# Performance work log

Measured on AMD Instinct MI355X. Metric: run time of the kernel, lower is better.

Reference implementation:

```python
import jax, jax.numpy as jnp
import numpy as np

B, S, E, H = 2, 2048, 1024, 16
D = E // H  # head_dim = 64
SCALE = D ** -0.5


def setup_inputs() -> dict:
    key = jax.random.key(0)
    ks = jax.random.split(key, 5)
    std = E ** -0.5
    return {
        "x": jax.random.normal(ks[0], (B, S, E), dtype=jnp.float32),
        "wq": jax.random.normal(ks[1], (E, E), dtype=jnp.float32) * std,
        "wk": jax.random.normal(ks[2], (E, E), dtype=jnp.float32) * std,
        "wv": jax.random.normal(ks[3], (E, E), dtype=jnp.float32) * std,
        "wo": jax.random.normal(ks[4], (E, E), dtype=jnp.float32) * std,
    }


def reference(x, wq, wk, wv, wo):
    b, s, e = x.shape
    # nn.Linear(bias=False): y = x @ W.T; then split heads -> [B,H,S,D]
    def heads(w):
        return jnp.einsum('bse,fe->bsf', x, w).reshape(b, s, H, D).transpose(0, 2, 1, 3)
    q, k, v = heads(wq), heads(wk), heads(wv)
    attn = jnp.einsum('bhqd,bhkd->bhqk', q, k) * SCALE  # [B,H,S,S]
    attn = jax.nn.softmax(attn, axis=-1)
    out = jnp.einsum('bhqk,bhkd->bhqd', attn, v)        # [B,H,S,D]
    out = out.transpose(0, 2, 1, 3).reshape(b, s, e)
    return jnp.einsum('bse,fe->bsf', out, wo)
```

## Files before the change

### kernel.cpp

```cpp
#include <hip/hip_runtime.h>
#include <stdint.h>

typedef unsigned short ushort_t;
typedef __bf16 bfx8 __attribute__((ext_vector_type(8), may_alias));
typedef __bf16 bfx2 __attribute__((ext_vector_type(2), may_alias));
typedef unsigned short usx8 __attribute__((ext_vector_type(8), may_alias));
typedef unsigned int uix2 __attribute__((ext_vector_type(2), may_alias));
typedef unsigned int uix4 __attribute__((ext_vector_type(4), may_alias));
typedef float f32x4 __attribute__((ext_vector_type(4)));
typedef float f32x4m __attribute__((ext_vector_type(4), may_alias));
typedef float f32x16 __attribute__((ext_vector_type(16)));

#define BB 2
#define SS 2048
#define EE 1024
#define HH 16
#define DD 64
#define MM (BB * SS)
#define XN ((size_t)MM * EE)
#define WN ((size_t)EE * EE)
#define QSCALE 0.18033688011112042f

__device__ __forceinline__ unsigned short f2bf(float f) {
  unsigned int u = __builtin_bit_cast(unsigned int, f);
  u += 0x7fffu + ((u >> 16) & 1u);
  return (unsigned short)(u >> 16);
}

__device__ __forceinline__ usx8 cvt8(const float* p) {
  f32x4m a = *(const f32x4m*)p;
  f32x4m b = *(const f32x4m*)(p + 4);
  usx8 r;
  r[0] = f2bf(a[0]); r[1] = f2bf(a[1]); r[2] = f2bf(a[2]); r[3] = f2bf(a[3]);
  r[4] = f2bf(b[0]); r[5] = f2bf(b[1]); r[6] = f2bf(b[2]); r[7] = f2bf(b[3]);
  return r;
}

__device__ __forceinline__ unsigned int pk2(float lo, float hi) {
  bfx2 t;
  t[0] = (__bf16)lo;
  t[1] = (__bf16)hi;
  return __builtin_bit_cast(unsigned int, t);
}

__device__ __forceinline__ void gl_lds16(const ushort_t* g, ushort_t* l) {
  __builtin_amdgcn_global_load_lds(
      (const __attribute__((address_space(1))) unsigned int*)g,
      (__attribute__((address_space(3))) unsigned int*)l, 16, 0, 0);
}

__global__ __launch_bounds__(256)
void cvt_qkv(const float* __restrict__ x, const float* __restrict__ wq,
             const float* __restrict__ wk, const float* __restrict__ wv,
             ushort_t* __restrict__ dst) {
  size_t i8 = ((size_t)blockIdx.x * 256 + threadIdx.x) * 8;
  const float* s;
  size_t off;
  if (i8 < XN)               { s = x;  off = i8; }
  else if (i8 < XN + WN)     { s = wq; off = i8 - XN; }
  else if (i8 < XN + 2 * WN) { s = wk; off = i8 - XN - WN; }
  else                       { s = wv; off = i8 - XN - 2 * WN; }
  *(usx8*)(dst + i8) = cvt8(s + off);
}

__global__ __launch_bounds__(256)
void cvt_one(const float* __restrict__ s, ushort_t* __restrict__ dst) {
  size_t i8 = ((size_t)blockIdx.x * 256 + threadIdx.x) * 8;
  *(usx8*)(dst + i8) = cvt8(s + i8);
}

__global__ __launch_bounds__(256)
void gemm_qkv(const ushort_t* __restrict__ xb,
              const ushort_t* __restrict__ wqb, const ushort_t* __restrict__ wkb,
              const ushort_t* __restrict__ wvb,
              ushort_t* __restrict__ Qb, ushort_t* __restrict__ Kb,
              ushort_t* __restrict__ Vtb) {
  __shared__ ushort_t As[128 * 32];
  __shared__ ushort_t Bs[128 * 32];

  const int bid = blockIdx.x;
  const ushort_t *A, *W;
  ushort_t* C;
  int bx, by, N;
  float scale = 1.0f;
  if (bid < 512) {
    int t = bid & 255;
    bx = t & 7;  by = t >> 3;
    A = xb;  N = EE;
    if (bid < 256) { W = wqb; C = Qb; scale = QSCALE; }
    else           { W = wkb; C = Kb; }
  } else {
    int t = bid - 512;
    bx = t & 31; by = t >> 5;
    A = wvb; W = xb; C = Vtb; N = MM;
  }
  const int K = EE;

  const int tid = threadIdx.x;
  const int lane = tid & 63;
  const int w = tid >> 6;
  const int l15 = lane & 15, l16 = lane >> 4;
  const int m0 = by * 128;
  const int n0 = bx * 128;
  const int wr = w >> 1, wc = w & 1;

  f32x4 acc[4][4];
#pragma unroll
  for (int i = 0; i < 4; ++i)
#pragma unroll
    for (int j = 0; j < 4; ++j)
#pragma unroll
      for (int r = 0; r < 4; ++r) acc[i][j][r] = 0.0f;

  for (int k0 = 0; k0 < K; k0 += 32) {
#pragma unroll
    for (int q = 0; q < 2; ++q) {
      int c = w * 128 + q * 64 + lane;
      int row = c >> 2, col = c & 3;
      gl_lds16(A + (size_t)(m0 + row) * K + k0 + col * 8,
               As + (size_t)(w * 128 + q * 64) * 8);
      gl_lds16(W + (size_t)(n0 + row) * K + k0 + col * 8,
               Bs + (size_t)(w * 128 + q * 64) * 8);
    }
    __syncthreads();

    bfx8 af[4], bfr[4];
#pragma unroll
    for (int i = 0; i < 4; ++i) {
      int mr = wr * 64 + i * 16 + l15;
      af[i] = *(const bfx8*)(As + mr * 32 + l16 * 8);
      int nr = wc * 64 + i * 16 + l15;
      bfr[i] = *(const bfx8*)(Bs + nr * 32 + l16 * 8);
    }
#pragma unroll
    for (int i = 0; i < 4; ++i)
#pragma unroll
      for (int j = 0; j < 4; ++j)
        acc[i][j] = __builtin_amdgcn_mfma_f32_16x16x32_bf16(af[i], bfr[j],
                                                            acc[i][j], 0, 0, 0);
    __syncthreads();
  }

#pragma unroll
  for (int i = 0; i < 4; ++i) {
    int mr = m0 + wr * 64 + i * 16 + l16 * 4;
#pragma unroll
    for (int j = 0; j < 4; ++j) {
      int nc = n0 + wc * 64 + j * 16 + l15;
#pragma unroll
      for (int r = 0; r < 4; ++r)
        C[(size_t)(mr + r) * N + nc] = f2bf(acc[i][j][r] * scale);
    }
  }
}

__global__ __launch_bounds__(256)
void gemm_o(const ushort_t* __restrict__ A, const ushort_t* __restrict__ W,
            float* __restrict__ C, int M, int N, int K) {
  __shared__ ushort_t As[128 * 32];
  __shared__ ushort_t Bs[128 * 32];

  const int tid = threadIdx.x;
  const int lane = tid & 63;
  const int w = tid >> 6;
  const int l15 = lane & 15, l16 = lane >> 4;
  const int m0 = blockIdx.y * 128;
  const int n0 = blockIdx.x * 128;
  const int wr = w >> 1, wc = w & 1;

  f32x4 acc[4][4];
#pragma unroll
  for (int i = 0; i < 4; ++i)
#pragma unroll
    for (int j = 0; j < 4; ++j)
#pragma unroll
      for (int r = 0; r < 4; ++r) acc[i][j][r] = 0.0f;

  for (int k0 = 0; k0 < K; k0 += 32) {
#pragma unroll
    for (int q = 0; q < 2; ++q) {
      int c = w * 128 + q * 64 + lane;
      int row = c >> 2, col = c & 3;
      gl_lds16(A + (size_t)(m0 + row) * K + k0 + col * 8,
               As + (size_t)(w * 128 + q * 64) * 8);
      gl_lds16(W + (size_t)(n0 + row) * K + k0 + col * 8,
               Bs + (size_t)(w * 128 + q * 64) * 8);
    }
    __syncthreads();

    bfx8 af[4], bfr[4];
#pragma unroll
    for (int i = 0; i < 4; ++i) {
      int mr = wr * 64 + i * 16 + l15;
      af[i] = *(const bfx8*)(As + mr * 32 + l16 * 8);
      int nr = wc * 64 + i * 16 + l15;
      bfr[i] = *(const bfx8*)(Bs + nr * 32 + l16 * 8);
    }
#pragma unroll
    for (int i = 0; i < 4; ++i)
#pragma unroll
      for (int j = 0; j < 4; ++j)
        acc[i][j] = __builtin_amdgcn_mfma_f32_16x16x32_bf16(af[i], bfr[j],
                                                            acc[i][j], 0, 0, 0);
    __syncthreads();
  }

#pragma unroll
  for (int i = 0; i < 4; ++i) {
    int mr = m0 + wr * 64 + i * 16 + l16 * 4;
#pragma unroll
    for (int j = 0; j < 4; ++j) {
      int nc = n0 + wc * 64 + j * 16 + l15;
#pragma unroll
      for (int r = 0; r < 4; ++r)
        C[(size_t)(mr + r) * N + nc] = acc[i][j][r];
    }
  }
}

__global__ __launch_bounds__(128)
void attn_fwd(const ushort_t* Q, const ushort_t* __restrict__ Kg,
              const ushort_t* __restrict__ Vt_g, ushort_t* AO) {
  __shared__ ushort_t Ks[64 * 72];
  __shared__ ushort_t Vs[64 * 72];

  const int tid = threadIdx.x;
  const int lane = tid & 63;
  const int w = tid >> 6;
  const int l31 = lane & 31, hi = lane >> 5;
  const int qt = blockIdx.x, h = blockIdx.y, b = blockIdx.z;
  const int q0 = qt * 64 + w * 32;

  bfx8 bq[4];
#pragma unroll
  for (int t = 0; t < 4; ++t)
    bq[t] = *(const bfx8*)(Q + (size_t)(b * SS + q0 + l31) * EE + h * DD +
                           t * 16 + hi * 8);

  f32x16 o0, o1;
#pragma unroll
  for (int r = 0; r < 16; ++r) { o0[r] = 0.0f; o1[r] = 0.0f; }
  float lsum = 0.0f;

  int cr[4], cc[4];
#pragma unroll
  for (int i = 0; i < 4; ++i) {
    int c = tid + i * 128;
    cr[i] = c >> 3;
    cc[i] = c & 7;
  }
  const ushort_t* kbase = Kg + (size_t)b * SS * EE + h * DD;
  const ushort_t* vbase = Vt_g + (size_t)h * DD * MM + (size_t)b * SS;

  usx8 kreg[4], vreg[4];
#pragma unroll
  for (int i = 0; i < 4; ++i) {
    kreg[i] = *(const usx8*)(kbase + (size_t)cr[i] * EE + cc[i] * 8);
    vreg[i] = *(const usx8*)(vbase + (size_t)cr[i] * MM + cc[i] * 8);
  }

  for (int kt = 0; kt < SS; kt += 64) {
    __syncthreads();
#pragma unroll
    for (int i = 0; i < 4; ++i) {
      *(usx8*)(Ks + cr[i] * 72 + cc[i] * 8) = kreg[i];
      *(usx8*)(Vs + cr[i] * 72 + cc[i] * 8) = vreg[i];
    }
    __syncthreads();
    if (kt + 64 < SS) {
#pragma unroll
      for (int i = 0; i < 4; ++i) {
        kreg[i] =
            *(const usx8*)(kbase + (size_t)(kt + 64 + cr[i]) * EE + cc[i] * 8);
        vreg[i] =
            *(const usx8*)(vbase + (size_t)cr[i] * MM + kt + 64 + cc[i] * 8);
      }
    }

    f32x16 pa, pb;
#pragma unroll
    for (int r = 0; r < 16; ++r) { pa[r] = 0.0f; pb[r] = 0.0f; }
#pragma unroll
    for (int t = 0; t < 4; ++t) {
      bfx8 ak0 = *(const bfx8*)(Ks + l31 * 72 + t * 16 + hi * 8);
      bfx8 ak1 = *(const bfx8*)(Ks + (32 + l31) * 72 + t * 16 + hi * 8);
      pa = __builtin_amdgcn_mfma_f32_32x32x16_bf16(ak0, bq[t], pa, 0, 0, 0);
      pb = __builtin_amdgcn_mfma_f32_32x32x16_bf16(ak1, bq[t], pb, 0, 0, 0);
    }

#pragma unroll
    for (int r = 0; r < 16; ++r) {
      pa[r] = __builtin_exp2f(pa[r]);
      pb[r] = __builtin_exp2f(pb[r]);
      lsum += pa[r] + pb[r];
    }

    unsigned int dwA[8], dwB[8];
#pragma unroll
    for (int s = 0; s < 8; ++s) {
      dwA[s] = pk2(pa[2 * s], pa[2 * s + 1]);
      dwB[s] = pk2(pb[2 * s], pb[2 * s + 1]);
    }
    bfx8 fd[4];
#pragma unroll
    for (int g = 0; g < 2; ++g) {
      auto sA = __builtin_amdgcn_permlane32_swap(dwA[4 * g + 0], dwA[4 * g + 2],
                                                 false, false);
      auto sB = __builtin_amdgcn_permlane32_swap(dwA[4 * g + 1], dwA[4 * g + 3],
                                                 false, false);
      uix4 f;
      f[0] = sA[0]; f[1] = sB[0]; f[2] = sA[1]; f[3] = sB[1];
      fd[g] = __builtin_bit_cast(bfx8, f);
      auto tA = __builtin_amdgcn_permlane32_swap(dwB[4 * g + 0], dwB[4 * g + 2],
                                                 false, false);
      auto tB = __builtin_amdgcn_permlane32_swap(dwB[4 * g + 1], dwB[4 * g + 3],
                                                 false, false);
      uix4 f2;
      f2[0] = tA[0]; f2[1] = tB[0]; f2[2] = tA[1]; f2[3] = tB[1];
      fd[2 + g] = __builtin_bit_cast(bfx8, f2);
    }

#pragma unroll
    for (int kk = 0; kk < 4; ++kk) {
      bfx8 av0 = *(const bfx8*)(Vs + l31 * 72 + kk * 16 + hi * 8);
      bfx8 av1 = *(const bfx8*)(Vs + (32 + l31) * 72 + kk * 16 + hi * 8);
      o0 = __builtin_amdgcn_mfma_f32_32x32x16_bf16(av0, fd[kk], o0, 0, 0, 0);
      o1 = __builtin_amdgcn_mfma_f32_32x32x16_bf16(av1, fd[kk], o1, 0, 0, 0);
    }
  }

  lsum += __shfl_xor(lsum, 32);
  float inv = 1.0f / lsum;

  ushort_t* orow = AO + (size_t)(b * SS + q0 + l31) * EE + h * DD;
#pragma unroll
  for (int g = 0; g < 4; ++g) {
    uix2 s0, s1;
    s0[0] = pk2(o0[4 * g + 0] * inv, o0[4 * g + 1] * inv);
    s0[1] = pk2(o0[4 * g + 2] * inv, o0[4 * g + 3] * inv);
    *(uix2*)(orow + 8 * g + 4 * hi) = s0;
    s1[0] = pk2(o1[4 * g + 0] * inv, o1[4 * g + 1] * inv);
    s1[1] = pk2(o1[4 * g + 2] * inv, o1[4 * g + 3] * inv);
    *(uix2*)(orow + 32 + 8 * g + 4 * hi) = s1;
  }
}

extern "C" void kernel_launch(void* const* d_in, const int* in_sizes, int n_in,
                              void* d_out, int out_size, void* d_ws, size_t ws_size,
                              hipStream_t stream) {
  const float* x  = (const float*)d_in[0];
  const float* wq = (const float*)d_in[1];
  const float* wk = (const float*)d_in[2];
  const float* wv = (const float*)d_in[3];
  const float* wo = (const float*)d_in[4];
  float* out = (float*)d_out;

  ushort_t* Qb  = (ushort_t*)d_ws;
  ushort_t* Kb  = Qb + XN;
  ushort_t* Vtb = Kb + XN;
  ushort_t* Ab  = Qb;
  ushort_t* S    = (ushort_t*)d_out;
  ushort_t* xb   = S;
  ushort_t* wqb  = S + XN;
  ushort_t* wkb  = S + XN + WN;
  ushort_t* wvb  = S + XN + 2 * WN;
  ushort_t* wob  = Kb;

  dim3 blk(256);
  cvt_qkv<<<dim3((unsigned)((XN + 3 * WN) / (256 * 8))), blk, 0, stream>>>(
      x, wq, wk, wv, S);
  gemm_qkv<<<dim3(768), blk, 0, stream>>>(xb, wqb, wkb, wvb, Qb, Kb, Vtb);
  attn_fwd<<<dim3(SS / 64, HH, BB), dim3(128), 0, stream>>>(Qb, Kb, Vtb, Ab);
  cvt_one<<<dim3((unsigned)(WN / (256 * 8))), blk, 0, stream>>>(wo, wob);
  gemm_o<<<dim3(EE / 128, MM / 128), blk, 0, stream>>>(
      Ab, wob, out, MM, EE, EE);
}
```

Measured before the change: 212.4 us.

## Load attention K/V fragments directly from global memory, dropping LDS staging

```diff
diff --git a/kernel.cpp b/kernel.cpp
--- a/kernel.cpp
+++ b/kernel.cpp
@@ -218,18 +218,16 @@
   }
 }
 
-__global__ __launch_bounds__(128)
+__global__ __launch_bounds__(64)
 void attn_fwd(const ushort_t* Q, const ushort_t* __restrict__ Kg,
               const ushort_t* __restrict__ Vt_g, ushort_t* AO) {
-  __shared__ ushort_t Ks[64 * 72];
-  __shared__ ushort_t Vs[64 * 72];
-
-  const int tid = threadIdx.x;
-  const int lane = tid & 63;
-  const int w = tid >> 6;
+  const int lane = threadIdx.x;
   const int l31 = lane & 31, hi = lane >> 5;
   const int qt = blockIdx.x, h = blockIdx.y, b = blockIdx.z;
-  const int q0 = qt * 64 + w * 32;
+  const int q0 = qt * 32;
+
+  const ushort_t* kbase = Kg + (size_t)b * SS * EE + h * DD;
+  const ushort_t* vbase = Vt_g + (size_t)h * DD * MM + (size_t)b * SS;
 
   bfx8 bq[4];
 #pragma unroll
@@ -242,39 +240,23 @@
   for (int r = 0; r < 16; ++r) { o0[r] = 0.0f; o1[r] = 0.0f; }
   float lsum = 0.0f;
 
-  int cr[4], cc[4];
-#pragma unroll
-  for (int i = 0; i < 4; ++i) {
-    int c = tid + i * 128;
-    cr[i] = c >> 3;
-    cc[i] = c & 7;
-  }
-  const ushort_t* kbase = Kg + (size_t)b * SS * EE + h * DD;
-  const ushort_t* vbase = Vt_g + (size_t)h * DD * MM + (size_t)b * SS;
-
-  usx8 kreg[4], vreg[4];
-#pragma unroll
-  for (int i = 0; i < 4; ++i) {
-    kreg[i] = *(const usx8*)(kbase + (size_t)cr[i] * EE + cc[i] * 8);
-    vreg[i] = *(const usx8*)(vbase + (size_t)cr[i] * MM + cc[i] * 8);
-  }
+  const ushort_t* kp0 = kbase + (size_t)l31 * EE + hi * 8;
+  const ushort_t* kp1 = kbase + (size_t)(32 + l31) * EE + hi * 8;
+  const ushort_t* vp0 = vbase + (size_t)l31 * MM + hi * 8;
+  const ushort_t* vp1 = vbase + (size_t)(32 + l31) * MM + hi * 8;
 
   for (int kt = 0; kt < SS; kt += 64) {
-    __syncthreads();
-#pragma unroll
-    for (int i = 0; i < 4; ++i) {
-      *(usx8*)(Ks + cr[i] * 72 + cc[i] * 8) = kreg[i];
-      *(usx8*)(Vs + cr[i] * 72 + cc[i] * 8) = vreg[i];
-    }
-    __syncthreads();
-    if (kt + 64 < SS) {
-#pragma unroll
-      for (int i = 0; i < 4; ++i) {
-        kreg[i] =
-            *(const usx8*)(kbase + (size_t)(kt + 64 + cr[i]) * EE + cc[i] * 8);
-        vreg[i] =
-            *(const usx8*)(vbase + (size_t)cr[i] * MM + kt + 64 + cc[i] * 8);
-      }
+    bfx8 ak0[4], ak1[4];
+#pragma unroll
+    for (int t = 0; t < 4; ++t) {
+      ak0[t] = *(const bfx8*)(kp0 + (size_t)kt * EE + t * 16);
+      ak1[t] = *(const bfx8*)(kp1 + (size_t)kt * EE + t * 16);
+    }
+    bfx8 av0[4], av1[4];
+#pragma unroll
+    for (int kk = 0; kk < 4; ++kk) {
+      av0[kk] = *(const bfx8*)(vp0 + kt + kk * 16);
+      av1[kk] = *(const bfx8*)(vp1 + kt + kk * 16);
     }
 
     f32x16 pa, pb;
@@ -282,10 +264,8 @@
     for (int r = 0; r < 16; ++r) { pa[r] = 0.0f; pb[r] = 0.0f; }
 #pragma unroll
     for (int t = 0; t < 4; ++t) {
-      bfx8 ak0 = *(const bfx8*)(Ks + l31 * 72 + t * 16 + hi * 8);
-      bfx8 ak1 = *(const bfx8*)(Ks + (32 + l31) * 72 + t * 16 + hi * 8);
-      pa = __builtin_amdgcn_mfma_f32_32x32x16_bf16(ak0, bq[t], pa, 0, 0, 0);
-      pb = __builtin_amdgcn_mfma_f32_32x32x16_bf16(ak1, bq[t], pb, 0, 0, 0);
+      pa = __builtin_amdgcn_mfma_f32_32x32x16_bf16(ak0[t], bq[t], pa, 0, 0, 0);
+      pb = __builtin_amdgcn_mfma_f32_32x32x16_bf16(ak1[t], bq[t], pb, 0, 0, 0);
     }
 
 #pragma unroll
@@ -322,10 +302,8 @@
 
 #pragma unroll
     for (int kk = 0; kk < 4; ++kk) {
-      bfx8 av0 = *(const bfx8*)(Vs + l31 * 72 + kk * 16 + hi * 8);
-      bfx8 av1 = *(const bfx8*)(Vs + (32 + l31) * 72 + kk * 16 + hi * 8);
-      o0 = __builtin_amdgcn_mfma_f32_32x32x16_bf16(av0, fd[kk], o0, 0, 0, 0);
-      o1 = __builtin_amdgcn_mfma_f32_32x32x16_bf16(av1, fd[kk], o1, 0, 0, 0);
+      o0 = __builtin_amdgcn_mfma_f32_32x32x16_bf16(av0[kk], fd[kk], o0, 0, 0, 0);
+      o1 = __builtin_amdgcn_mfma_f32_32x32x16_bf16(av1[kk], fd[kk], o1, 0, 0, 0);
     }
   }
 
@@ -370,7 +348,7 @@
   cvt_qkv<<<dim3((unsigned)((XN + 3 * WN) / (256 * 8))), blk, 0, stream>>>(
       x, wq, wk, wv, S);
   gemm_qkv<<<dim3(768), blk, 0, stream>>>(xb, wqb, wkb, wvb, Qb, Kb, Vtb);
-  attn_fwd<<<dim3(SS / 64, HH, BB), dim3(128), 0, stream>>>(Qb, Kb, Vtb, Ab);
+  attn_fwd<<<dim3(SS / 32, HH, BB), dim3(64), 0, stream>>>(Qb, Kb, Vtb, Ab);
   cvt_one<<<dim3((unsigned)(WN / (256 * 8))), blk, 0, stream>>>(wo, wob);
   gemm_o<<<dim3(EE / 128, MM / 128), blk, 0, stream>>>(
       Ab, wob, out, MM, EE, EE);
```

After: 263.9 us. +24.3%, slower.

## Run attention with single-wave blocks, XCD-aware grid mapping and MFMA priority hints

Applied to the files above, without the earlier changes.

```diff
diff --git a/kernel.cpp b/kernel.cpp
--- a/kernel.cpp
+++ b/kernel.cpp
@@ -7,6 +7,7 @@
 typedef unsigned short usx8 __attribute__((ext_vector_type(8), may_alias));
 typedef unsigned int uix2 __attribute__((ext_vector_type(2), may_alias));
 typedef unsigned int uix4 __attribute__((ext_vector_type(4), may_alias));
+typedef float f32x2 __attribute__((ext_vector_type(2)));
 typedef float f32x4 __attribute__((ext_vector_type(4)));
 typedef float f32x4m __attribute__((ext_vector_type(4), may_alias));
 typedef float f32x16 __attribute__((ext_vector_type(16)));
@@ -218,18 +219,23 @@
   }
 }
 
-__global__ __launch_bounds__(128)
+__global__ __launch_bounds__(64, 2)
 void attn_fwd(const ushort_t* Q, const ushort_t* __restrict__ Kg,
               const ushort_t* __restrict__ Vt_g, ushort_t* AO) {
   __shared__ ushort_t Ks[64 * 72];
   __shared__ ushort_t Vs[64 * 72];
 
-  const int tid = threadIdx.x;
-  const int lane = tid & 63;
-  const int w = tid >> 6;
+  const int lane = threadIdx.x;
   const int l31 = lane & 31, hi = lane >> 5;
-  const int qt = blockIdx.x, h = blockIdx.y, b = blockIdx.z;
-  const int q0 = qt * 64 + w * 32;
+  const int n = blockIdx.x;
+  const int xcd = n & 7, rr = n >> 3;
+  const int g = xcd * 4 + (rr >> 6);
+  const int qt = rr & 63;
+  const int h = g & 15, b = g >> 4;
+  const int q0 = qt * 32;
+
+  const ushort_t* kbase = Kg + (size_t)b * SS * EE + h * DD;
+  const ushort_t* vbase = Vt_g + (size_t)h * DD * MM + (size_t)b * SS;
 
   bfx8 bq[4];
 #pragma unroll
@@ -240,46 +246,38 @@
   f32x16 o0, o1;
 #pragma unroll
   for (int r = 0; r < 16; ++r) { o0[r] = 0.0f; o1[r] = 0.0f; }
-  float lsum = 0.0f;
-
-  int cr[4], cc[4];
-#pragma unroll
-  for (int i = 0; i < 4; ++i) {
-    int c = tid + i * 128;
-    cr[i] = c >> 3;
-    cc[i] = c & 7;
-  }
-  const ushort_t* kbase = Kg + (size_t)b * SS * EE + h * DD;
-  const ushort_t* vbase = Vt_g + (size_t)h * DD * MM + (size_t)b * SS;
-
-  usx8 kreg[4], vreg[4];
-#pragma unroll
-  for (int i = 0; i < 4; ++i) {
-    kreg[i] = *(const usx8*)(kbase + (size_t)cr[i] * EE + cc[i] * 8);
-    vreg[i] = *(const usx8*)(vbase + (size_t)cr[i] * MM + cc[i] * 8);
+  f32x2 ls2;
+  ls2[0] = 0.0f; ls2[1] = 0.0f;
+
+  const int srow = lane >> 3, scol = lane & 7;
+
+  usx8 kreg[8], vreg[8];
+#pragma unroll
+  for (int i = 0; i < 8; ++i) {
+    kreg[i] = *(const usx8*)(kbase + (size_t)(srow + 8 * i) * EE + scol * 8);
+    vreg[i] = *(const usx8*)(vbase + (size_t)(srow + 8 * i) * MM + scol * 8);
   }
 
   for (int kt = 0; kt < SS; kt += 64) {
-    __syncthreads();
-#pragma unroll
-    for (int i = 0; i < 4; ++i) {
-      *(usx8*)(Ks + cr[i] * 72 + cc[i] * 8) = kreg[i];
-      *(usx8*)(Vs + cr[i] * 72 + cc[i] * 8) = vreg[i];
-    }
-    __syncthreads();
+#pragma unroll
+    for (int i = 0; i < 8; ++i) {
+      *(usx8*)(Ks + (srow + 8 * i) * 72 + scol * 8) = kreg[i];
+      *(usx8*)(Vs + (srow + 8 * i) * 72 + scol * 8) = vreg[i];
+    }
     if (kt + 64 < SS) {
 #pragma unroll
-      for (int i = 0; i < 4; ++i) {
-        kreg[i] =
-            *(const usx8*)(kbase + (size_t)(kt + 64 + cr[i]) * EE + cc[i] * 8);
-        vreg[i] =
-            *(const usx8*)(vbase + (size_t)cr[i] * MM + kt + 64 + cc[i] * 8);
+      for (int i = 0; i < 8; ++i) {
+        kreg[i] = *(const usx8*)(kbase + (size_t)(kt + 64 + srow + 8 * i) * EE +
+                                 scol * 8);
+        vreg[i] = *(const usx8*)(vbase + (size_t)(srow + 8 * i) * MM + kt + 64 +
+                                 scol * 8);
       }
     }
 
     f32x16 pa, pb;
 #pragma unroll
     for (int r = 0; r < 16; ++r) { pa[r] = 0.0f; pb[r] = 0.0f; }
+    __builtin_amdgcn_s_setprio(1);
 #pragma unroll
     for (int t = 0; t < 4; ++t) {
       bfx8 ak0 = *(const bfx8*)(Ks + l31 * 72 + t * 16 + hi * 8);
@@ -287,12 +285,19 @@
       pa = __builtin_amdgcn_mfma_f32_32x32x16_bf16(ak0, bq[t], pa, 0, 0, 0);
       pb = __builtin_amdgcn_mfma_f32_32x32x16_bf16(ak1, bq[t], pb, 0, 0, 0);
     }
+    __builtin_amdgcn_s_setprio(0);
 
 #pragma unroll
     for (int r = 0; r < 16; ++r) {
       pa[r] = __builtin_exp2f(pa[r]);
       pb[r] = __builtin_exp2f(pb[r]);
-      lsum += pa[r] + pb[r];
+    }
+#pragma unroll
+    for (int s = 0; s < 8; ++s) {
+      f32x2 ta, tb;
+      ta[0] = pa[2 * s]; ta[1] = pa[2 * s + 1];
+      tb[0] = pb[2 * s]; tb[1] = pb[2 * s + 1];
+      ls2 += ta + tb;
     }
 
     unsigned int dwA[8], dwB[8];
@@ -303,23 +308,24 @@
     }
     bfx8 fd[4];
 #pragma unroll
-    for (int g = 0; g < 2; ++g) {
-      auto sA = __builtin_amdgcn_permlane32_swap(dwA[4 * g + 0], dwA[4 * g + 2],
-                                                 false, false);
-      auto sB = __builtin_amdgcn_permlane32_swap(dwA[4 * g + 1], dwA[4 * g + 3],
-                                                 false, false);
+    for (int g2 = 0; g2 < 2; ++g2) {
+      auto sA = __builtin_amdgcn_permlane32_swap(dwA[4 * g2 + 0],
+                                                 dwA[4 * g2 + 2], false, false);
+      auto sB = __builtin_amdgcn_permlane32_swap(dwA[4 * g2 + 1],
+                                                 dwA[4 * g2 + 3], false, false);
       uix4 f;
       f[0] = sA[0]; f[1] = sB[0]; f[2] = sA[1]; f[3] = sB[1];
-      fd[g] = __builtin_bit_cast(bfx8, f);
-      auto tA = __builtin_amdgcn_permlane32_swap(dwB[4 * g + 0], dwB[4 * g + 2],
-                                                 false, false);
-      auto tB = __builtin_amdgcn_permlane32_swap(dwB[4 * g + 1], dwB[4 * g + 3],
-                                                 false, false);
+      fd[g2] = __builtin_bit_cast(bfx8, f);
+      auto tA = __builtin_amdgcn_permlane32_swap(dwB[4 * g2 + 0],
+                                                 dwB[4 * g2 + 2], false, false);
+      auto tB = __builtin_amdgcn_permlane32_swap(dwB[4 * g2 + 1],
+                                                 dwB[4 * g2 + 3], false, false);
       uix4 f2;
       f2[0] = tA[0]; f2[1] = tB[0]; f2[2] = tA[1]; f2[3] = tB[1];
-      fd[2 + g] = __builtin_bit_cast(bfx8, f2);
-    }
-
+      fd[2 + g2] = __builtin_bit_cast(bfx8, f2);
+    }
+
+    __builtin_amdgcn_s_setprio(1);
 #pragma unroll
     for (int kk = 0; kk < 4; ++kk) {
       bfx8 av0 = *(const bfx8*)(Vs + l31 * 72 + kk * 16 + hi * 8);
@@ -327,21 +333,23 @@
       o0 = __builtin_amdgcn_mfma_f32_32x32x16_bf16(av0, fd[kk], o0, 0, 0, 0);
       o1 = __builtin_amdgcn_mfma_f32_32x32x16_bf16(av1, fd[kk], o1, 0, 0, 0);
     }
-  }
-
+    __builtin_amdgcn_s_setprio(0);
+  }
+
+  float lsum = ls2[0] + ls2[1];
   lsum += __shfl_xor(lsum, 32);
   float inv = 1.0f / lsum;
 
   ushort_t* orow = AO + (size_t)(b * SS + q0 + l31) * EE + h * DD;
 #pragma unroll
-  for (int g = 0; g < 4; ++g) {
+  for (int g2 = 0; g2 < 4; ++g2) {
     uix2 s0, s1;
-    s0[0] = pk2(o0[4 * g + 0] * inv, o0[4 * g + 1] * inv);
-    s0[1] = pk2(o0[4 * g + 2] * inv, o0[4 * g + 3] * inv);
-    *(uix2*)(orow + 8 * g + 4 * hi) = s0;
-    s1[0] = pk2(o1[4 * g + 0] * inv, o1[4 * g + 1] * inv);
-    s1[1] = pk2(o1[4 * g + 2] * inv, o1[4 * g + 3] * inv);
-    *(uix2*)(orow + 32 + 8 * g + 4 * hi) = s1;
+    s0[0] = pk2(o0[4 * g2 + 0] * inv, o0[4 * g2 + 1] * inv);
+    s0[1] = pk2(o0[4 * g2 + 2] * inv, o0[4 * g2 + 3] * inv);
+    *(uix2*)(orow + 8 * g2 + 4 * hi) = s0;
+    s1[0] = pk2(o1[4 * g2 + 0] * inv, o1[4 * g2 + 1] * inv);
+    s1[1] = pk2(o1[4 * g2 + 2] * inv, o1[4 * g2 + 3] * inv);
+    *(uix2*)(orow + 32 + 8 * g2 + 4 * hi) = s1;
   }
 }
 
@@ -370,7 +378,7 @@
   cvt_qkv<<<dim3((unsigned)((XN + 3 * WN) / (256 * 8))), blk, 0, stream>>>(
       x, wq, wk, wv, S);
   gemm_qkv<<<dim3(768), blk, 0, stream>>>(xb, wqb, wkb, wvb, Qb, Kb, Vtb);
-  attn_fwd<<<dim3(SS / 64, HH, BB), dim3(128), 0, stream>>>(Qb, Kb, Vtb, Ab);
+  attn_fwd<<<dim3(2048), dim3(64), 0, stream>>>(Qb, Kb, Vtb, Ab);
   cvt_one<<<dim3((unsigned)(WN / (256 * 8))), blk, 0, stream>>>(wo, wob);
   gemm_o<<<dim3(EE / 128, MM / 128), blk, 0, stream>>>(
       Ab, wob, out, MM, EE, EE);
```

Result: no change. 212.7 us (+0.2%).
